# Kernel tuning notes

Hardware: AMD Instinct MI355X
Metric: run time of the kernel (lower is better)

## Reference

```python
import jax, jax.numpy as jnp
import numpy as np
from jax import lax

KERNEL = 21
SHIFT = KERNEL - 1  # 20
NUM_LEVELS = 2
EPS = 1e-5
NEG_SLOPE = 0.01


def _conv1d(x, w):
    # x: [B, Cin, T], w: [Cout, Cin, K] -> [B, Cout, T-K+1]
    return lax.conv_general_dilated(x, w, window_strides=(1,), padding='VALID',
                                    dimension_numbers=('NCH', 'OIH', 'NCH'))


def _batchnorm_train(x, gamma, beta):
    # training-mode BN over (N, L) per channel, biased variance (torch semantics)
    mean = jnp.mean(x, axis=(0, 2), keepdims=True)
    var = jnp.mean((x - mean) ** 2, axis=(0, 2), keepdims=True)
    return (x - mean) * lax.rsqrt(var + EPS) * gamma[None, :, None] + beta[None, :, None]


def _spp(y, L, num_levels, pool):
    # y: [B, C, Tc]; L: [B] valid lengths. Level i has 2^i bins:
    #   bin j covers [j*floor(L/2^i), j*floor(L/2^i)+ceil(L/2^i)), matching
    #   F.max_pool1d/avg_pool1d(kernel=ceil(f), stride=floor(f)) on x[:, :, :L].
    B, C, Tc = y.shape
    pos = jnp.arange(Tc)[None, :]                     # [1, Tc]
    Lf = L.astype(jnp.float32)
    outs = []
    for i in range(num_levels):
        k = 2 ** i
        f = Lf / k
        stride = jnp.floor(f).astype(jnp.int32)        # [B]
        kern = jnp.ceil(f).astype(jnp.int32)           # [B]
        bins = []
        for j in range(k):
            start = j * stride                         # [B]
            mask = (pos >= start[:, None]) & (pos < (start + kern)[:, None])  # [B, Tc]
            m = mask[:, None, :]                       # [B, 1, Tc]
            if pool == 'max':
                bins.append(jnp.max(jnp.where(m, y, -jnp.inf), axis=-1))      # [B, C]
            else:
                s = jnp.sum(jnp.where(m, y, jnp.zeros((), y.dtype)), axis=-1)
                bins.append(s / kern[:, None].astype(y.dtype))
        # torch .view flattens (C, k) channel-major
        outs.append(jnp.stack(bins, axis=-1).reshape(B, C * k))
    return jnp.concatenate(outs, axis=1)               # [B, C*(2^n - 1)]


def setup_inputs() -> dict:
    key = jax.random.key(0)
    k1, k2, k3, k4, k5 = jax.random.split(key, 5)
    B, C, T = 32, 64, 16384
    n_tasks = 2
    n_lin = 2 * C * (2 ** NUM_LEVELS - 1)  # 384
    x = jax.random.normal(k1, (B, C, T), dtype=jnp.float32)
    orig_len = jax.random.randint(k2, (B,), T // 2, T + 1, dtype=jnp.int32)
    w1 = jax.random.normal(k3, (C, C, KERNEL), dtype=jnp.float32) * 0.05
    w2 = jax.random.normal(k4, (C, C, KERNEL), dtype=jnp.float32) * 0.05
    g1 = jnp.ones((C,), jnp.float32); b1 = jnp.zeros((C,), jnp.float32)
    g2 = jnp.ones((C,), jnp.float32); b2 = jnp.zeros((C,), jnp.float32)
    fc_w = jax.random.normal(k5, (n_tasks, n_lin), dtype=jnp.float32) * 0.05
    fc_b = jnp.zeros((n_tasks,), jnp.float32)
    return {"x": x, "orig_len": orig_len, "w1": w1, "g1": g1, "b1": b1,
            "w2": w2, "g2": g2, "b2": b2, "fc_w": fc_w, "fc_b": fc_b}


def reference(x, orig_len, w1, g1, b1, w2, g2, b2, fc_w, fc_b):
    L = orig_len - SHIFT  # valid conv-output length per sample
    y1 = jax.nn.leaky_relu(_batchnorm_train(_conv1d(x, w1), g1, b1), NEG_SLOPE)
    p1 = _spp(y1, L, NUM_LEVELS, 'max')
    y2 = jax.nn.leaky_relu(_batchnorm_train(_conv1d(x, w2), g2, b2), NEG_SLOPE)
    p2 = _spp(y2, L, NUM_LEVELS, 'avg')
    feat = jnp.concatenate([p1, p2], axis=1)           # [B, 384]
    return feat @ fc_w.T + fc_b
```

## Files before the change

### kernel.cpp

```cpp
#include <hip/hip_runtime.h>

#define AS1 __attribute__((address_space(1)))
#define AS3 __attribute__((address_space(3)))

using u16 = unsigned short;
using u32 = unsigned int;
typedef __attribute__((ext_vector_type(8))) short bf16x8;
typedef __attribute__((ext_vector_type(4))) float f32x4;

constexpr int Bn    = 32;
constexpr int Tn    = 16384;
constexpr int TCn   = 16364;
constexpr int TILE  = 256;
constexpr int XROWS = 280;
constexpr int TPAD  = 16416;

__device__ __forceinline__ u16 f2bf(float f) {
  union { float f; u32 u; } v; v.f = f;
  u32 u = v.u;
  u += 0x7fffu + ((u >> 16) & 1u);
  return (u16)(u >> 16);
}
__device__ __forceinline__ float bf2f(u32 h) {
  union { u32 u; float f; } v; v.u = h << 16; return v.f;
}
__device__ __forceinline__ u32 encf(float f) {
  union { float f; u32 u; } v; v.f = f;
  return (v.u & 0x80000000u) ? ~v.u : (v.u | 0x80000000u);
}
__device__ __forceinline__ float decf(u32 u) {
  union { u32 u; float f; } v;
  v.u = (u & 0x80000000u) ? (u ^ 0x80000000u) : ~u;
  return v.f;
}
__device__ __forceinline__ void gload_lds16(const void* g, void* l) {
  __builtin_amdgcn_global_load_lds((const AS1 u32*)g, (AS3 u32*)l, 16, 0, 0);
}
__device__ __forceinline__ float leaky(float z) { return z > 0.f ? z : 0.01f * z; }

__global__ __launch_bounds__(256) void transpose_x(const float* __restrict__ x,
                                                   u16* __restrict__ x_t,
                                                   const float* __restrict__ w1,
                                                   const float* __restrict__ w2,
                                                   u16* __restrict__ wf1,
                                                   u16* __restrict__ wf2) {
  __shared__ u16 lt[64][64];
  const int bx  = blockIdx.x;
  const int tid = threadIdx.x;

  if (bx >= Bn * 256) {
    const int bxx = bx - Bn * 256;
    const int cv  = bxx / 42;
    const int c   = bxx % 42;
    const float* w = cv ? w2 : w1;
    u16* wf = cv ? wf2 : wf1;
    const int ct   = tid >> 6;
    const int lane = tid & 63;
    const int q  = lane >> 4;
    const int rr = lane & 15;
    const int k  = c >> 1;
    const int cb = (c & 1) * 32;
    const int co = ct * 16 + rr;
    u16 us[8] __attribute__((aligned(16)));
#pragma unroll
    for (int j = 0; j < 8; ++j) {
      int ci = cb + q * 8 + j;
      us[j] = f2bf(w[((size_t)co * 64 + ci) * 21 + k]);
    }
    *(uint4*)&wf[((size_t)(c * 4 + ct) * 64 + lane) * 8] = *(const uint4*)us;
    return;
  }

  const int b   = bx >> 8;
  const int tt  = bx & 255;
  const int t0  = tt * 64;
  const int ci0 = (tid & 15) * 4;
  const int tl0 = (tid >> 4) * 4;
  float4 v[4];
#pragma unroll
  for (int j = 0; j < 4; ++j)
    v[j] = *(const float4*)(x + (size_t)(b * 64 + ci0 + j) * Tn + t0 + tl0);
  float vr[4][4] = {{v[0].x,v[0].y,v[0].z,v[0].w},{v[1].x,v[1].y,v[1].z,v[1].w},
                    {v[2].x,v[2].y,v[2].z,v[2].w},{v[3].x,v[3].y,v[3].z,v[3].w}};
#pragma unroll
  for (int e = 0; e < 4; ++e) {
    int tl = tl0 + e;
    u32 lo = (u32)f2bf(vr[0][e]) | ((u32)f2bf(vr[1][e]) << 16);
    u32 hi = (u32)f2bf(vr[2][e]) | ((u32)f2bf(vr[3][e]) << 16);
    uint2 pk = make_uint2(lo, hi);
    *(uint2*)&lt[tl][ci0] = pk;
  }
  __syncthreads();
  const int row = tid >> 2;
  const int seg = tid & 3;
  const int c0  = seg * 16;
  const int sw  = (row & 7) * 8;
  u16* op = x_t + ((size_t)b * TPAD + t0 + row) * 64 + c0;
  *(uint4*)op       = *(const uint4*)&lt[row][c0 ^ sw];
  *(uint4*)(op + 8) = *(const uint4*)&lt[row][(c0 + 8) ^ sw];
  if (tt == 0) {
    uint4 z = make_uint4(0u, 0u, 0u, 0u);
    uint4* pz = (uint4*)(x_t + ((size_t)b * TPAD + Tn) * 64);
    pz[tid] = z;
  }
}

__global__ __launch_bounds__(256, 4) void conv_mfma(const u16* __restrict__ x_t,
                                                    const u16* __restrict__ wf1,
                                                    const u16* __restrict__ wf2,
                                                    u16* __restrict__ y1,
                                                    u16* __restrict__ y2,
                                                    float* __restrict__ stats) {
  __shared__ u16 xs[XROWS * 64];
  __shared__ float sred[128];

  const int bid  = blockIdx.x;
  const int cv   = bid & 1;
  const int tmp  = bid >> 1;
  const int tile = tmp & 63;
  const int b    = tmp >> 6;
  const int t0   = tile * TILE;
  const int tid  = threadIdx.x;
  const int w    = tid >> 6;
  const int lane = tid & 63;
  const int q    = lane >> 4;
  const int r    = lane & 15;
  const u16* wf  = cv ? wf2 : wf1;

  if (tid < 128) sred[tid] = 0.f;

  const u16* xg = x_t + ((size_t)b * TPAD + t0) * 64;
  for (int s = w; s < 35; s += 4)
    gload_lds16(xg + (size_t)s * 512 + lane * 8, &xs[s * 512]);

  const u16* wfl = wf + lane * 8;
  bf16x8 afA[4], afB[4];
#pragma unroll
  for (int ct = 0; ct < 4; ++ct) afA[ct] = *(const bf16x8*)(wfl + ct * 512);
#pragma unroll
  for (int ct = 0; ct < 4; ++ct) afB[ct] = *(const bf16x8*)(wfl + 2048 + ct * 512);

  __syncthreads();

  f32x4 acc[4][4];
#pragma unroll
  for (int a = 0; a < 4; ++a)
#pragma unroll
    for (int t = 0; t < 4; ++t)
      acc[a][t] = (f32x4){0.f, 0.f, 0.f, 0.f};

  const int rowbase = w * 64 + r;

  for (int j = 0; j < 21; ++j) {
    const int swl  = ((rowbase + j) & 7) * 8;
    const int cid0 = (q * 8) ^ swl;
    const int cid1 = cid0 ^ 32;
    {
      bf16x8 bx[4];
#pragma unroll
      for (int tt = 0; tt < 4; ++tt)
        bx[tt] = *(const bf16x8*)&xs[(rowbase + tt * 16 + j) * 64 + cid0];
      __builtin_amdgcn_s_setprio(1);
#pragma unroll
      for (int ct = 0; ct < 4; ++ct)
#pragma unroll
        for (int tt = 0; tt < 4; ++tt)
          acc[ct][tt] = __builtin_amdgcn_mfma_f32_16x16x32_bf16(afA[ct], bx[tt], acc[ct][tt], 0, 0, 0);
      __builtin_amdgcn_s_setprio(0);
      if (j < 20) {
        const u16* p = wfl + (size_t)(2 * j + 2) * 2048;
#pragma unroll
        for (int ct = 0; ct < 4; ++ct) afA[ct] = *(const bf16x8*)(p + ct * 512);
      }
    }
    {
      bf16x8 bx[4];
#pragma unroll
      for (int tt = 0; tt < 4; ++tt)
        bx[tt] = *(const bf16x8*)&xs[(rowbase + tt * 16 + j) * 64 + cid1];
      __builtin_amdgcn_s_setprio(1);
#pragma unroll
      for (int ct = 0; ct < 4; ++ct)
#pragma unroll
        for (int tt = 0; tt < 4; ++tt)
          acc[ct][tt] = __builtin_amdgcn_mfma_f32_16x16x32_bf16(afB[ct], bx[tt], acc[ct][tt], 0, 0, 0);
      __builtin_amdgcn_s_setprio(0);
      if (j < 20) {
        const u16* p = wfl + (size_t)(2 * j + 3) * 2048;
#pragma unroll
        for (int ct = 0; ct < 4; ++ct) afB[ct] = *(const bf16x8*)(p + ct * 512);
      }
    }
  }

  const bool full_t = (t0 + TILE <= TCn);
#pragma unroll
  for (int ct = 0; ct < 4; ++ct)
#pragma unroll
    for (int i = 0; i < 4; ++i) {
      float sv = 0.f, sq = 0.f;
      if (full_t) {
#pragma unroll
        for (int tt = 0; tt < 4; ++tt) {
          float v = acc[ct][tt][i];
          sv += v; sq += v * v;
        }
      } else {
#pragma unroll
        for (int tt = 0; tt < 4; ++tt) {
          int tg = t0 + w * 64 + tt * 16 + r;
          if (tg < TCn) {
            float v = acc[ct][tt][i];
            sv += v; sq += v * v;
          }
        }
      }
#pragma unroll
      for (int m = 1; m < 16; m <<= 1) {
        sv += __shfl_xor(sv, m, 64);
        sq += __shfl_xor(sq, m, 64);
      }
      if (r == 0) {
        int co = ct * 16 + q * 4 + i;
        atomicAdd(&sred[co * 2], sv);
        atomicAdd(&sred[co * 2 + 1], sq);
      }
    }

  __syncthreads();

  u16* ys = xs;
#pragma unroll
  for (int ct = 0; ct < 4; ++ct)
#pragma unroll
    for (int tt = 0; tt < 4; ++tt) {
      int tl = w * 64 + tt * 16 + r;
      int sw = (tl & 7) * 8;
      int co0 = (ct * 16 + q * 4) ^ sw;
      u32 lo = (u32)f2bf(acc[ct][tt][0]) | ((u32)f2bf(acc[ct][tt][1]) << 16);
      u32 hi = (u32)f2bf(acc[ct][tt][2]) | ((u32)f2bf(acc[ct][tt][3]) << 16);
      *(uint2*)&ys[tl * 64 + co0] = make_uint2(lo, hi);
    }
  __syncthreads();
  u16* yo = (cv ? y2 : y1) + ((size_t)b * Tn + t0) * 64;
#pragma unroll
  for (int m = 0; m < 8; ++m) {
    int flat = m * 256 + tid;
    int row  = flat >> 3;
    int c0   = (flat & 7) * 8;
    int sw   = (row & 7) * 8;
    *(uint4*)(yo + (size_t)row * 64 + c0) = *(const uint4*)&ys[row * 64 + (c0 ^ sw)];
  }
  if (tid < 128) atomicAdd(&stats[cv * 128 + tid], sred[tid]);
}

__global__ __launch_bounds__(256) void spp(const u16* __restrict__ y1,
                                           const u16* __restrict__ y2,
                                           const float* __restrict__ stats,
                                           const float* __restrict__ g1v,
                                           const float* __restrict__ b1v,
                                           const float* __restrict__ g2v,
                                           const float* __restrict__ b2v,
                                           const int* __restrict__ orig_len,
                                           u32* __restrict__ featU) {
  const int bx = blockIdx.x;
  const int b  = bx >> 4;
  const int ch = bx & 15;
  const int tid  = threadIdx.x;
  const int g    = tid & 15;
  const int trow = tid >> 4;
  const int co0  = g * 4;
  const int L     = orig_len[b] - 20;
  const int str2  = L >> 1;
  const int kern2 = L - str2;
  const float Nf = 32.0f * 16364.0f;
  float a1[4], c1[4], a2[4], c2[4];
#pragma unroll
  for (int j = 0; j < 4; ++j) {
    int co = co0 + j;
    float s, sq, mean, var;
    s = stats[co * 2]; sq = stats[co * 2 + 1];
    mean = s / Nf; var = sq / Nf - mean * mean; if (var < 0.f) var = 0.f;
    a1[j] = g1v[co] * rsqrtf(var + 1e-5f);
    c1[j] = b1v[co] - mean * a1[j];
    s = stats[128 + co * 2]; sq = stats[128 + co * 2 + 1];
    mean = s / Nf; var = sq / Nf - mean * mean; if (var < 0.f) var = 0.f;
    a2[j] = g2v[co] * rsqrtf(var + 1e-5f);
    c2[j] = b2v[co] - mean * a2[j];
  }
  float m1[4] = {-3.4e38f,-3.4e38f,-3.4e38f,-3.4e38f};
  float m2[4] = {-3.4e38f,-3.4e38f,-3.4e38f,-3.4e38f};
  float s0[4] = {0,0,0,0}, sb0[4] = {0,0,0,0}, sb1[4] = {0,0,0,0};
  const int tbase = ch * 1024;
  int tend = tbase + 1024;
  if (tend > L) tend = L;
  const u16* p1 = y1 + (size_t)b * Tn * 64 + co0;
  const u16* p2 = y2 + (size_t)b * Tn * 64 + co0;
  for (int t = tbase + trow; t < tend; t += 16) {
    uint2 v1 = *(const uint2*)(p1 + (size_t)t * 64);
    uint2 v2 = *(const uint2*)(p2 + (size_t)t * 64);
    float f1[4] = { bf2f(v1.x & 0xffffu), bf2f(v1.x >> 16),
                    bf2f(v1.y & 0xffffu), bf2f(v1.y >> 16) };
    float f2[4] = { bf2f(v2.x & 0xffffu), bf2f(v2.x >> 16),
                    bf2f(v2.y & 0xffffu), bf2f(v2.y >> 16) };
    bool in0 = (t < kern2), in1 = (t >= str2);
#pragma unroll
    for (int j = 0; j < 4; ++j) {
      float z1 = leaky(fmaf(a1[j], f1[j], c1[j]));
      float z2 = leaky(fmaf(a2[j], f2[j], c2[j]));
      s0[j] += z2;
      if (in0) { m1[j] = fmaxf(m1[j], z1); sb0[j] += z2; }
      if (in1) { m2[j] = fmaxf(m2[j], z1); sb1[j] += z2; }
    }
  }
#pragma unroll
  for (int m = 16; m <= 32; m <<= 1) {
#pragma unroll
    for (int j = 0; j < 4; ++j) {
      m1[j]  = fmaxf(m1[j], __shfl_xor(m1[j], m, 64));
      m2[j]  = fmaxf(m2[j], __shfl_xor(m2[j], m, 64));
      s0[j]  += __shfl_xor(s0[j],  m, 64);
      sb0[j] += __shfl_xor(sb0[j], m, 64);
      sb1[j] += __shfl_xor(sb1[j], m, 64);
    }
  }
  if (((tid & 63) >> 4) == 0) {
    u32* fb = featU + (size_t)b * 384;
    float* ff = (float*)fb;
#pragma unroll
    for (int j = 0; j < 4; ++j) {
      int co = co0 + j;
      u32 e1 = encf(m1[j]), e2 = encf(m2[j]);
      atomicMax(&fb[co], e1 > e2 ? e1 : e2);
      atomicMax(&fb[64 + co * 2], e1);
      atomicMax(&fb[64 + co * 2 + 1], e2);
      atomicAdd(&ff[192 + co], s0[j]);
      atomicAdd(&ff[256 + co * 2], sb0[j]);
      atomicAdd(&ff[256 + co * 2 + 1], sb1[j]);
    }
  }
}

__global__ void fc(const u32* __restrict__ featU,
                   const int* __restrict__ orig_len,
                   const float* __restrict__ fc_w,
                   const float* __restrict__ fc_b,
                   float* __restrict__ out) {
  const int tid  = threadIdx.x;
  const int pair = tid >> 2;
  const int part = tid & 3;
  const int b = pair >> 1;
  const int n = pair & 1;
  const int L = orig_len[b] - 20;
  const int kern2 = L - (L >> 1);
  const u32* fb = featU + (size_t)b * 384;
  const float* ff = (const float*)fb;
  float acc = 0.f;
  for (int j = part; j < 384; j += 4) {
    float fv;
    if (j < 192)      fv = decf(fb[j]);
    else if (j < 256) fv = ff[j] / (float)L;
    else              fv = ff[j] / (float)kern2;
    acc += fv * fc_w[n * 384 + j];
  }
  acc += __shfl_xor(acc, 1, 64);
  acc += __shfl_xor(acc, 2, 64);
  if (part == 0) out[b * 2 + n] = acc + fc_b[n];
}

extern "C" void kernel_launch(void* const* d_in, const int* in_sizes, int n_in,
                              void* d_out, int out_size, void* d_ws, size_t ws_size,
                              hipStream_t stream) {
  const float* x        = (const float*)d_in[0];
  const int*   orig_len = (const int*)d_in[1];
  const float* w1  = (const float*)d_in[2];
  const float* g1  = (const float*)d_in[3];
  const float* b1  = (const float*)d_in[4];
  const float* w2  = (const float*)d_in[5];
  const float* g2  = (const float*)d_in[6];
  const float* b2  = (const float*)d_in[7];
  const float* fcw = (const float*)d_in[8];
  const float* fcb = (const float*)d_in[9];
  float* out = (float*)d_out;

  char* ws = (char*)d_ws;
  const size_t XT_BYTES = (size_t)Bn * TPAD * 64 * 2;
  const size_t Y_BYTES  = (size_t)Bn * Tn * 64 * 2;
  const size_t WF_BYTES = (size_t)42 * 4 * 64 * 8 * 2;
  size_t off = 0;
  u16* x_t = (u16*)(ws + off); off += XT_BYTES;
  u16* y1  = (u16*)(ws + off); off += Y_BYTES;
  u16* y2  = (u16*)(ws + off); off += Y_BYTES;
  u16* wf1 = (u16*)(ws + off); off += WF_BYTES;
  u16* wf2 = (u16*)(ws + off); off += WF_BYTES;
  float* stats = (float*)(ws + off);
  u32*   featU = (u32*)(ws + off + 1024);
  const size_t SMALL_BYTES = 1024 + 49152;

  hipMemsetAsync(ws + off, 0, SMALL_BYTES, stream);
  transpose_x<<<Bn * 256 + 84, 256, 0, stream>>>(x, x_t, w1, w2, wf1, wf2);
  conv_mfma<<<Bn * 64 * 2, 256, 0, stream>>>(x_t, wf1, wf2, y1, y2, stats);
  spp<<<Bn * 16, 256, 0, stream>>>(y1, y2, stats, g1, b1, g2, b2, orig_len, featU);
  fc<<<1, 256, 0, stream>>>(featU, orig_len, fcw, fcb, out);
  (void)in_sizes; (void)n_in; (void)out_size; (void)ws_size;
}
```

Before: 466.1 us.

## Split SPP into finer chunks with per-block partials, parallelize FC reduction

The SPP kernel now uses 64 chunks of 256 timesteps per sample instead of 16 chunks of 1024, which gives four times as many blocks. Each block reduces its partial max/sum values in shared memory and writes them to a private partial buffer, replacing global atomics. The FC kernel then runs one block per sample, reduces the 64 partials itself and computes the dot product with wave shuffles. This removes atomic contention and the large memset, at the cost of an extra partial buffer read in the FC stage.

```diff
diff --git a/kernel.cpp b/kernel.cpp
--- a/kernel.cpp
+++ b/kernel.cpp
@@ -14,6 +14,7 @@
 constexpr int TILE  = 256;
 constexpr int XROWS = 280;
 constexpr int TPAD  = 16416;
+constexpr int SPPCH = 64;
 
 __device__ __forceinline__ u16 f2bf(float f) {
   union { float f; u32 u; } v; v.f = f;
@@ -262,13 +263,15 @@
                                            const float* __restrict__ g2v,
                                            const float* __restrict__ b2v,
                                            const int* __restrict__ orig_len,
-                                           u32* __restrict__ featU) {
+                                           u32* __restrict__ part) {
+  __shared__ float lred[4][16][4][5];
   const int bx = blockIdx.x;
-  const int b  = bx >> 4;
-  const int ch = bx & 15;
+  const int b  = bx >> 6;
+  const int ch = bx & 63;
   const int tid  = threadIdx.x;
   const int g    = tid & 15;
   const int trow = tid >> 4;
+  const int wv   = tid >> 6;
   const int co0  = g * 4;
   const int L     = orig_len[b] - 20;
   const int str2  = L >> 1;
@@ -291,12 +294,13 @@
   float m1[4] = {-3.4e38f,-3.4e38f,-3.4e38f,-3.4e38f};
   float m2[4] = {-3.4e38f,-3.4e38f,-3.4e38f,-3.4e38f};
   float s0[4] = {0,0,0,0}, sb0[4] = {0,0,0,0}, sb1[4] = {0,0,0,0};
-  const int tbase = ch * 1024;
-  int tend = tbase + 1024;
+  const int tbase = ch * 256;
+  int tend = tbase + 256;
   if (tend > L) tend = L;
   const u16* p1 = y1 + (size_t)b * Tn * 64 + co0;
   const u16* p2 = y2 + (size_t)b * Tn * 64 + co0;
-  for (int t = tbase + trow; t < tend; t += 16) {
+
+  auto body = [&](int t) {
     uint2 v1 = *(const uint2*)(p1 + (size_t)t * 64);
     uint2 v2 = *(const uint2*)(p2 + (size_t)t * 64);
     float f1[4] = { bf2f(v1.x & 0xffffu), bf2f(v1.x >> 16),
@@ -312,7 +316,17 @@
       if (in0) { m1[j] = fmaxf(m1[j], z1); sb0[j] += z2; }
       if (in1) { m2[j] = fmaxf(m2[j], z1); sb1[j] += z2; }
     }
-  }
+  };
+
+  if (tend == tbase + 256) {
+#pragma unroll 4
+    for (int it = 0; it < 16; ++it)
+      body(tbase + trow + it * 16);
+  } else {
+    for (int t = tbase + trow; t < tend; t += 16)
+      body(t);
+  }
+
 #pragma unroll
   for (int m = 16; m <= 32; m <<= 1) {
 #pragma unroll
@@ -325,47 +339,83 @@
     }
   }
   if (((tid & 63) >> 4) == 0) {
-    u32* fb = featU + (size_t)b * 384;
-    float* ff = (float*)fb;
 #pragma unroll
     for (int j = 0; j < 4; ++j) {
-      int co = co0 + j;
-      u32 e1 = encf(m1[j]), e2 = encf(m2[j]);
-      atomicMax(&fb[co], e1 > e2 ? e1 : e2);
-      atomicMax(&fb[64 + co * 2], e1);
-      atomicMax(&fb[64 + co * 2 + 1], e2);
-      atomicAdd(&ff[192 + co], s0[j]);
-      atomicAdd(&ff[256 + co * 2], sb0[j]);
-      atomicAdd(&ff[256 + co * 2 + 1], sb1[j]);
-    }
-  }
-}
-
-__global__ void fc(const u32* __restrict__ featU,
-                   const int* __restrict__ orig_len,
-                   const float* __restrict__ fc_w,
-                   const float* __restrict__ fc_b,
-                   float* __restrict__ out) {
-  const int tid  = threadIdx.x;
-  const int pair = tid >> 2;
-  const int part = tid & 3;
-  const int b = pair >> 1;
-  const int n = pair & 1;
+      lred[wv][g][j][0] = m1[j];
+      lred[wv][g][j][1] = m2[j];
+      lred[wv][g][j][2] = s0[j];
+      lred[wv][g][j][3] = sb0[j];
+      lred[wv][g][j][4] = sb1[j];
+    }
+  }
+  __syncthreads();
+  if (tid < 64) {
+    const int co = tid;
+    const int g2 = co >> 2, j2 = co & 3;
+    float fm1 = lred[0][g2][j2][0], fm2 = lred[0][g2][j2][1];
+    float fs0 = lred[0][g2][j2][2], fb0 = lred[0][g2][j2][3], fb1v_ = lred[0][g2][j2][4];
+#pragma unroll
+    for (int k = 1; k < 4; ++k) {
+      fm1 = fmaxf(fm1, lred[k][g2][j2][0]);
+      fm2 = fmaxf(fm2, lred[k][g2][j2][1]);
+      fs0 += lred[k][g2][j2][2];
+      fb0 += lred[k][g2][j2][3];
+      fb1v_ += lred[k][g2][j2][4];
+    }
+    u32* pp = part + (size_t)bx * 384;
+    float* pf = (float*)pp;
+    u32 e1 = encf(fm1), e2 = encf(fm2);
+    pp[co]              = e1 > e2 ? e1 : e2;
+    pp[64 + co * 2]     = e1;
+    pp[64 + co * 2 + 1] = e2;
+    pf[192 + co]         = fs0;
+    pf[256 + co * 2]     = fb0;
+    pf[256 + co * 2 + 1] = fb1v_;
+  }
+}
+
+__global__ __launch_bounds__(384) void fc(const u32* __restrict__ part,
+                                          const int* __restrict__ orig_len,
+                                          const float* __restrict__ fc_w,
+                                          const float* __restrict__ fc_b,
+                                          float* __restrict__ out) {
+  __shared__ float r0s[6], r1s[6];
+  const int b = blockIdx.x;
+  const int j = threadIdx.x;
   const int L = orig_len[b] - 20;
   const int kern2 = L - (L >> 1);
-  const u32* fb = featU + (size_t)b * 384;
-  const float* ff = (const float*)fb;
-  float acc = 0.f;
-  for (int j = part; j < 384; j += 4) {
-    float fv;
-    if (j < 192)      fv = decf(fb[j]);
-    else if (j < 256) fv = ff[j] / (float)L;
-    else              fv = ff[j] / (float)kern2;
-    acc += fv * fc_w[n * 384 + j];
-  }
-  acc += __shfl_xor(acc, 1, 64);
-  acc += __shfl_xor(acc, 2, 64);
-  if (part == 0) out[b * 2 + n] = acc + fc_b[n];
+  const u32* pb = part + (size_t)b * 64 * 384;
+  float fv;
+  if (j < 192) {
+    u32 vmax = 0u;
+    for (int c = 0; c < 64; ++c) {
+      u32 v = pb[(size_t)c * 384 + j];
+      vmax = v > vmax ? v : vmax;
+    }
+    fv = decf(vmax);
+  } else {
+    const float* pf = (const float*)pb;
+    float s = 0.f;
+    for (int c = 0; c < 64; ++c) s += pf[(size_t)c * 384 + j];
+    fv = (j < 256) ? s / (float)L : s / (float)kern2;
+  }
+  float a0 = fv * fc_w[j];
+  float a1 = fv * fc_w[384 + j];
+#pragma unroll
+  for (int m = 1; m < 64; m <<= 1) {
+    a0 += __shfl_xor(a0, m, 64);
+    a1 += __shfl_xor(a1, m, 64);
+  }
+  const int wv = j >> 6, ln = j & 63;
+  if (ln == 0) { r0s[wv] = a0; r1s[wv] = a1; }
+  __syncthreads();
+  if (j == 0) {
+    float t0 = 0.f, t1 = 0.f;
+#pragma unroll
+    for (int k = 0; k < 6; ++k) { t0 += r0s[k]; t1 += r1s[k]; }
+    out[b * 2]     = t0 + fc_b[0];
+    out[b * 2 + 1] = t1 + fc_b[1];
+  }
 }
 
 extern "C" void kernel_launch(void* const* d_in, const int* in_sizes, int n_in,
@@ -394,13 +444,12 @@
   u16* wf1 = (u16*)(ws + off); off += WF_BYTES;
   u16* wf2 = (u16*)(ws + off); off += WF_BYTES;
   float* stats = (float*)(ws + off);
-  u32*   featU = (u32*)(ws + off + 1024);
-  const size_t SMALL_BYTES = 1024 + 49152;
-
-  hipMemsetAsync(ws + off, 0, SMALL_BYTES, stream);
+  u32*   part  = (u32*)(ws + off + 1024);
+
+  hipMemsetAsync(stats, 0, 1024, stream);
   transpose_x<<<Bn * 256 + 84, 256, 0, stream>>>(x, x_t, w1, w2, wf1, wf2);
   conv_mfma<<<Bn * 64 * 2, 256, 0, stream>>>(x_t, wf1, wf2, y1, y2, stats);
-  spp<<<Bn * 16, 256, 0, stream>>>(y1, y2, stats, g1, b1, g2, b2, orig_len, featU);
-  fc<<<1, 256, 0, stream>>>(featU, orig_len, fcw, fcb, out);
+  spp<<<Bn * SPPCH, 256, 0, stream>>>(y1, y2, stats, g1, b1, g2, b2, orig_len, part);
+  fc<<<Bn, 384, 0, stream>>>(part, orig_len, fcw, fcb, out);
   (void)in_sizes; (void)n_in; (void)out_size; (void)ws_size;
 }
```

Result: faster. 395.1 us (-15.2%).
